# Kernel optimization log

Measured on AMD Instinct MI355X. Metric: run time of the kernel, lower is better.

Reference implementation:

```python
import jax, jax.numpy as jnp
import numpy as np

BS, HIST, H, W, NOBJ = 512, 3, 10, 10, 4
NSENT, TOK, DM = 3, 36, 768
EMB, FM, K, NL, ADIM = 256, 64, 2, 128, 5
LIN = FM * (H - (K - 1)) * (W - (K - 1))  # 64*9*9 = 5184
ATTN_SCALE = float(np.sqrt(EMB))  # 16.0


def setup_inputs() -> dict:
    key = jax.random.key(0)
    ks = jax.random.split(key, 24)
    g = lambda i, shape, s=0.02: jax.random.normal(ks[i], shape, dtype=jnp.float32) * s
    sprite_emb = g(0, (25, EMB), 1.0).at[0].set(0.0)  # padding_idx=0 -> zero row
    inp = {
        'state': jax.random.randint(ks[1], (BS, HIST, H, W, NOBJ), 0, 25, dtype=jnp.int32),
        'action': jax.random.randint(ks[2], (BS,), 0, ADIM, dtype=jnp.int32),
        'temb': jax.random.normal(ks[3], (BS, NSENT, TOK, DM), dtype=jnp.float32),
        'sprite_emb': sprite_emb,
        'conv_w': g(4, (K, K, HIST * EMB, FM)),  # HWIO
        'conv_b': g(5, (FM,)),
        'Wk': g(6, (DM, EMB)), 'bk': g(7, (EMB,)),
        'Wks': g(8, (DM, 1)), 'bks': g(9, (1,)),
        'Wv': g(10, (DM, EMB)), 'bv': g(11, (EMB,)),
        'Wvs': g(12, (DM, 1)), 'bvs': g(13, (1,)),
        'a1': g(14, (LIN, NL)), 'a1b': g(15, (NL,)),
        'a2': g(16, (NL, NL)), 'a2b': g(17, (NL,)),
        'a3': g(18, (NL, ADIM)), 'a3b': g(19, (ADIM,)),
        'v1': g(20, (LIN, NL)), 'v1b': g(21, (NL,)),
        'v2': g(22, (NL, NL)), 'v2b': g(23, (NL,)),
        'v3': jax.random.normal(jax.random.fold_in(key, 99), (NL, 1)) * 0.02,
        'v3b': jnp.zeros((1,), jnp.float32),
    }
    return inp


def _nonzero_mean(e):
    # e: [..., n, emb]; mean over rows that are nonzero (padding rows are all-zero)
    cnt = jnp.sum(jnp.sum(e, axis=-1) != 0, axis=-1, keepdims=True)
    return jnp.sum(e, axis=-2) / jnp.maximum(cnt, 1).astype(e.dtype)


def reference(state, action, temb, sprite_emb, conv_w, conv_b, Wk, bk, Wks, bks,
              Wv, bv, Wvs, bvs, a1, a1b, a2, a2b, a3, a3b, v1, v1b, v2, v2b, v3, v3b):
    lrelu = jax.nn.leaky_relu  # slope 0.01 matches torch default
    bs = state.shape[0]
    obj_state, avt_state = state[..., :-1], state[..., -1:]
    query = _nonzero_mean(sprite_emb[obj_state])   # [bs,hist,H,W,emb]
    avatar = _nonzero_mean(sprite_emb[avt_state])  # [bs,hist,H,W,emb]
    # text key/value: scaled token-softmax pooling over tokens (dim=2)
    k = (temb @ Wk + bk) * jax.nn.softmax(temb @ Wks + bks, axis=-2)
    k = jnp.sum(k, axis=2)                          # [bs,nsent,emb]
    v = (temb @ Wv + bv) * jax.nn.softmax(temb @ Wvs + bvs, axis=-2)
    v = jnp.sum(v, axis=2)                          # [bs,nsent,emb]
    # batch_attention
    q2 = query.reshape(bs, -1, EMB)                 # [bs, hist*H*W, emb]
    kq = jnp.einsum('bxe,bse->bxs', q2, k) / ATTN_SCALE
    wts = jax.nn.softmax(kq, axis=-1) * (kq != 0)
    wts = wts.reshape(bs, HIST, H, W, NSENT)
    # mean(weights[...,None]*value, dim=-2) == (w @ v) / nsent
    att = jnp.einsum('bthws,bse->bthwe', wts, v) / NSENT  # [bs,hist,H,W,emb]
    st = att.reshape(bs, H, W, -1)                  # fold hist into channels (768)
    av = avatar.reshape(bs, H, W, -1)
    st = (st + av) / 2.0                            # NHWC, C=768
    y = jax.lax.conv_general_dilated(st, conv_w, (1, 1), 'VALID',
                                     dimension_numbers=('NHWC', 'HWIO', 'NHWC')) + conv_b
    y = lrelu(y)                                    # [bs,9,9,64]
    y = jnp.transpose(y, (0, 3, 1, 2)).reshape(bs, -1)  # torch NCHW flatten order
    ha = lrelu(lrelu(y @ a1 + a1b) @ a2 + a2b)
    logits = ha @ a3 + a3b
    logp = jax.nn.log_softmax(logits, axis=-1)
    action_logprobs = jnp.take_along_axis(logp, action[:, None].astype(jnp.int32), axis=-1)[:, 0]
    entropy = -jnp.sum(jnp.exp(logp) * logp, axis=-1)
    hv = lrelu(lrelu(y @ v1 + v1b) @ v2 + v2b)
    state_value = (hv @ v3 + v3b)[:, 0]
    return action_logprobs, state_value, entropy
```

## Files before the change

kernel.cpp:

```cpp
#include <hip/hip_runtime.h>
#include <hip/hip_bf16.h>
#include <math.h>

constexpr int BS   = 512;
constexpr int DM   = 768;
constexpr int NBS  = 1536;
constexpr int NPOS = 300;
constexpr int LIN  = 5184;
constexpr int KSPLIT = 27, KCH = 192;

typedef __attribute__((ext_vector_type(8))) short bf16x8;
typedef __attribute__((ext_vector_type(4))) short s16x4;
typedef __attribute__((ext_vector_type(4))) float f32x4;

static __device__ __forceinline__ short f2bf(float f) {
    unsigned u = __float_as_uint(f);
    unsigned r = (u + 0x7FFFu + ((u >> 16) & 1u)) >> 16;
    return (short)r;
}

constexpr size_t OFF_P    = 0;
constexpr size_t OFF_C0   = 19200;
constexpr size_t OFF_FL   = 19264;
constexpr size_t OFF_RD   = 19328;
constexpr size_t OFF_DT   = 39296;
constexpr size_t OFF_W2T  = 77696;
constexpr size_t OFF_WVH  = 176000;
constexpr size_t OFF_WCT  = 274304;
constexpr size_t OFF_AB   = 569216;
constexpr size_t OFF_SK   = 1232768;
constexpr size_t OFF_SV   = 1288064;
constexpr size_t OFF_XVH  = 1343360;
constexpr size_t OFF_VW   = 1933184;
constexpr size_t OFF_YH   = 3112832;
constexpr size_t OFF_PART = 4439936;

__global__ __launch_bounds__(256) void kA_prep(
    const float* __restrict__ conv_w, const float* __restrict__ sprite,
    const float* __restrict__ bk, const float* __restrict__ Wk,
    const float* __restrict__ Wv, const float* __restrict__ bv,
    const float* __restrict__ a1, const float* __restrict__ v1,
    short* __restrict__ W2T, short* __restrict__ WVH, short* __restrict__ AB,
    float* __restrict__ P, float* __restrict__ RD,
    float* __restrict__ C0, int* __restrict__ FL)
{
    __shared__ float tile[64][65];
    int bx = blockIdx.x, tid = threadIdx.x;
    if (bx < 48) {
        int p = bx >> 2, cq = bx & 3;
        int t4 = p / 3, j = p - t4 * 3;
        int c0 = cq * 64;
        #pragma unroll
        for (int it = 0; it < 16; ++it) {
            int idx = it * 256 + tid; int ci = idx >> 6, f = idx & 63;
            tile[ci][f] = conv_w[(size_t)(t4 * 768 + j * 256 + c0 + ci) * 64 + f];
        }
        __syncthreads();
        #pragma unroll
        for (int it = 0; it < 16; ++it) {
            int idx = it * 256 + tid; int f = idx >> 6, ci = idx & 63;
            W2T[(size_t)((t4 * 3 + j) * 64 + f) * 256 + c0 + ci] = f2bf(tile[ci][f]);
        }
    } else if (bx < 96) {
        int id = bx - 48;
        int base = id * 4096 + tid * 16;
        #pragma unroll
        for (int q = 0; q < 4; ++q) {
            float4 v = *(const float4*)(Wv + base + q * 4);
            s16x4 h = { f2bf(v.x), f2bf(v.y), f2bf(v.z), f2bf(v.w) };
            *(s16x4*)(WVH + base + q * 4) = h;
        }
    } else if (bx < 420) {
        int id = bx - 96; int kt = id % 81, nt = id / 81;
        const float* src = (nt < 2) ? a1 : v1;
        int col0 = (nt & 1) * 64;
        #pragma unroll
        for (int it = 0; it < 16; ++it) {
            int idx = it * 256 + tid; int ki = idx >> 6, ni = idx & 63;
            tile[ki][ni] = src[(size_t)(kt * 64 + ki) * 128 + col0 + ni];
        }
        __syncthreads();
        #pragma unroll
        for (int it = 0; it < 16; ++it) {
            int idx = it * 256 + tid; int ni = idx >> 6, ki = idx & 63;
            AB[(size_t)(nt * 64 + ni) * 5184 + kt * 64 + ki] = f2bf(tile[ki][ni]);
        }
    } else if (bx < 495) {
        int g = (bx - 420) * 256 + tid; int o = g / 768, d = g - o * 768;
        const float* sp = sprite + o * 256;
        const float* wr = Wk + (size_t)d * 256;
        float s = 0.f;
        for (int c = 0; c < 256; ++c) s += sp[c] * wr[c];
        P[g] = s;
    } else if (bx < 573) {
        int g = (bx - 495) * 256 + tid;
        int o = g / 768, n = g - o * 768;
        int tap = n >> 6, f = n & 63; int t4 = tap / 3, j = tap - t4 * 3;
        const float* sp = (o < 25) ? (sprite + o * 256) : bv;
        float s = 0.f;
        for (int e = 0; e < 256; ++e)
            s += sp[e] * conv_w[(size_t)(t4 * 768 + j * 256 + e) * 64 + f];
        RD[g] = s;
    } else {
        if (tid < 25) {
            float s = 0.f, cc = 0.f;
            for (int c = 0; c < 256; ++c) {
                float e = sprite[tid * 256 + c];
                s += e; cc += e * bk[c];
            }
            FL[tid] = (s != 0.0f) ? 1 : 0;
            C0[tid] = cc;
        }
    }
}

__global__ __launch_bounds__(256) void kB1_scores(
    const float* __restrict__ temb, const float* __restrict__ Wks,
    const float* __restrict__ Wvs, float* __restrict__ SK, float* __restrict__ SV)
{
    int wid = threadIdx.x >> 6, lane = threadIdx.x & 63;
    int r = blockIdx.x * 4 + wid;
    const float4* row = (const float4*)temb + (size_t)r * 192;
    const float4* k4 = (const float4*)Wks;
    const float4* v4 = (const float4*)Wvs;
    float pk = 0.f, pv = 0.f;
    #pragma unroll
    for (int i = 0; i < 3; ++i) {
        int d4 = lane + 64 * i;
        float4 x = row[d4];
        float4 wk = k4[d4], wv = v4[d4];
        pk += x.x * wk.x + x.y * wk.y + x.z * wk.z + x.w * wk.w;
        pv += x.x * wv.x + x.y * wv.y + x.z * wv.z + x.w * wv.w;
    }
    #pragma unroll
    for (int off = 32; off; off >>= 1) {
        pk += __shfl_down(pk, off);
        pv += __shfl_down(pv, off);
    }
    if (lane == 0) { SK[r] = pk; SV[r] = pv; }
}

__global__ __launch_bounds__(256) void kB2_sum(
    const float* __restrict__ temb, const float* __restrict__ SK,
    const float* __restrict__ SV, const float* __restrict__ P,
    const float* __restrict__ C0, short* __restrict__ XVH, float* __restrict__ DT)
{
    __shared__ float swk[40], swv[40];
    __shared__ float xk[768], xv[768];
    int tid = threadIdx.x, wid = tid >> 6, lane = tid & 63;
    int bs = blockIdx.x;

    if (wid < 2) {
        const float* S = wid ? SV : SK;
        float s = (lane < 36) ? S[bs * 36 + lane] : -INFINITY;
        float m = s;
        #pragma unroll
        for (int off = 32; off; off >>= 1) m = fmaxf(m, __shfl_xor(m, off));
        float e = (lane < 36) ? expf(s - m) : 0.f;
        float z = e;
        #pragma unroll
        for (int off = 32; off; off >>= 1) z += __shfl_xor(z, off);
        float* dst = wid ? swv : swk;
        if (lane < 36) dst[lane] = e / z;
    }
    __syncthreads();

    int tl[3], dd[3];
    #pragma unroll
    for (int i = 0; i < 3; ++i) { int g = i * 256 + tid; tl[i] = g / 192; dd[i] = g % 192; }
    float4 accK[3], accV[3];
    #pragma unroll
    for (int i = 0; i < 3; ++i) {
        accK[i] = make_float4(0.f, 0.f, 0.f, 0.f);
        accV[i] = make_float4(0.f, 0.f, 0.f, 0.f);
    }
    const float4* row = (const float4*)temb + (size_t)bs * 6912;
    for (int g = 0; g < 9; ++g) {
        #pragma unroll
        for (int i = 0; i < 3; ++i) {
            float4 x = row[g * 768 + i * 256 + tid];
            float wk = swk[4 * g + tl[i]], wv = swv[4 * g + tl[i]];
            accK[i].x += wk * x.x; accK[i].y += wk * x.y;
            accK[i].z += wk * x.z; accK[i].w += wk * x.w;
            accV[i].x += wv * x.x; accV[i].y += wv * x.y;
            accV[i].z += wv * x.z; accV[i].w += wv * x.w;
        }
    }
    #pragma unroll
    for (int p = 0; p < 4; ++p) {
        #pragma unroll
        for (int i = 0; i < 3; ++i) if (tl[i] == p) {
            if (p == 0) {
                *(float4*)&xk[4 * dd[i]] = accK[i];
                *(float4*)&xv[4 * dd[i]] = accV[i];
            } else {
                float4 t0 = *(const float4*)&xk[4 * dd[i]];
                t0.x += accK[i].x; t0.y += accK[i].y; t0.z += accK[i].z; t0.w += accK[i].w;
                *(float4*)&xk[4 * dd[i]] = t0;
                float4 t1 = *(const float4*)&xv[4 * dd[i]];
                t1.x += accV[i].x; t1.y += accV[i].y; t1.z += accV[i].z; t1.w += accV[i].w;
                *(float4*)&xv[4 * dd[i]] = t1;
            }
        }
        __syncthreads();
    }
    if (tid < 192) {
        float4 vv = *(const float4*)&xv[4 * tid];
        s16x4 h = { f2bf(vv.x), f2bf(vv.y), f2bf(vv.z), f2bf(vv.w) };
        *(s16x4*)(XVH + (size_t)bs * 768 + 4 * tid) = h;
    }
    for (int o = wid; o < 25; o += 4) {
        const float* pr = P + o * 768;
        float s = 0.f;
        #pragma unroll
        for (int j = 0; j < 12; ++j) s += xk[lane + 64 * j] * pr[lane + 64 * j];
        #pragma unroll
        for (int off = 32; off; off >>= 1) s += __shfl_down(s, off);
        if (lane == 0) DT[bs * 25 + o] = s + C0[o];
    }
}

template<int BIAS, int OUTBF>
__global__ __launch_bounds__(256) void gemm_mfma(
    const short* __restrict__ A, const short* __restrict__ B,
    const float* __restrict__ bias, void* __restrict__ Cout,
    int K, int ldc, int klen, size_t czstride)
{
    __shared__ short As[64][40];
    __shared__ short Bs[64][40];
    int tid = threadIdx.x;
    int bm = blockIdx.x * 64, bn = blockIdx.y * 64;
    int wid = tid >> 6, lane = tid & 63;
    int wm = (wid >> 1) * 32, wn = (wid & 1) * 32;
    int l15 = lane & 15, lg = lane >> 4;

    f32x4 zero = {0.f, 0.f, 0.f, 0.f};
    f32x4 acc00 = zero, acc01 = zero, acc10 = zero, acc11 = zero;

    int srow = tid >> 2, kch = (tid & 3) * 8;
    const short* Ap = A + (size_t)(bm + srow) * K + kch + (size_t)blockIdx.z * klen;
    const short* Bp = B + (size_t)(bn + srow) * K + kch + (size_t)blockIdx.z * klen;

    for (int kt = 0; kt < klen; kt += 32) {
        bf16x8 aval = *(const bf16x8*)(Ap + kt);
        bf16x8 bval = *(const bf16x8*)(Bp + kt);
        *(bf16x8*)&As[srow][kch] = aval;
        *(bf16x8*)&Bs[srow][kch] = bval;
        __syncthreads();
        bf16x8 af0 = *(const bf16x8*)&As[wm + l15][lg * 8];
        bf16x8 af1 = *(const bf16x8*)&As[wm + 16 + l15][lg * 8];
        bf16x8 bg0 = *(const bf16x8*)&Bs[wn + l15][lg * 8];
        bf16x8 bg1 = *(const bf16x8*)&Bs[wn + 16 + l15][lg * 8];
        acc00 = __builtin_amdgcn_mfma_f32_16x16x32_bf16(af0, bg0, acc00, 0, 0, 0);
        acc01 = __builtin_amdgcn_mfma_f32_16x16x32_bf16(af0, bg1, acc01, 0, 0, 0);
        acc10 = __builtin_amdgcn_mfma_f32_16x16x32_bf16(af1, bg0, acc10, 0, 0, 0);
        acc11 = __builtin_amdgcn_mfma_f32_16x16x32_bf16(af1, bg1, acc11, 0, 0, 0);
        __syncthreads();
    }

    float* Cf = (float*)Cout + (size_t)blockIdx.z * czstride;
    short* Ch = (short*)Cout;
    #pragma unroll
    for (int i = 0; i < 2; ++i) {
        f32x4 arow0 = (i == 0) ? acc00 : acc10;
        f32x4 arow1 = (i == 0) ? acc01 : acc11;
        #pragma unroll
        for (int j = 0; j < 2; ++j) {
            f32x4 a = (j == 0) ? arow0 : arow1;
            int col = bn + wn + j * 16 + l15;
            float bb = BIAS ? bias[col] : 0.f;
            #pragma unroll
            for (int r = 0; r < 4; ++r) {
                int row = bm + wm + i * 16 + lg * 4 + r;
                float v = a[r] + bb;
                if (OUTBF) Ch[(size_t)row * ldc + col] = f2bf(v);
                else       Cf[(size_t)row * ldc + col] = v;
            }
        }
    }
}

__global__ __launch_bounds__(256) void k4_y(
    const int* __restrict__ state, const float* __restrict__ dt,
    const int* __restrict__ flags, const float* __restrict__ vW,
    const float* __restrict__ rowdot, const float* __restrict__ conv_b,
    short* __restrict__ y)
{
    int b = blockIdx.x, tid = threadIdx.x;
    __shared__ float s_vW[3 * 768];
    __shared__ float s_w[3][NPOS + 4];
    __shared__ int   s_avt[NPOS + 4];
    __shared__ float s_y[81 * 65];

    const float4* vs = (const float4*)(vW + (size_t)b * 3 * 768);
    float4* vd = (float4*)s_vW;
    for (int i = tid; i < 576; i += 256) vd[i] = vs[i];

    for (int code = tid; code < NPOS; code += 256) {
        const int* st = state + ((size_t)b * NPOS + code) * 4;
        int o0 = st[0], o1 = st[1], o2 = st[2], avi = st[3];
        int cnt = flags[o0] + flags[o1] + flags[o2];
        s_avt[code] = avi;
        float w0 = 0.f, w1 = 0.f, w2 = 0.f;
        if (cnt > 0) {
            const float* d0 = dt + (size_t)b * 75;
            float inv = 1.0f / (16.0f * (float)cnt);
            float q0 = (d0[o0]      + d0[o1]      + d0[o2])      * inv;
            float q1 = (d0[25 + o0] + d0[25 + o1] + d0[25 + o2]) * inv;
            float q2 = (d0[50 + o0] + d0[50 + o1] + d0[50 + o2]) * inv;
            float m = fmaxf(q0, fmaxf(q1, q2));
            float e0 = expf(q0 - m), e1 = expf(q1 - m), e2 = expf(q2 - m);
            float is = 1.0f / (6.0f * (e0 + e1 + e2));
            w0 = e0 * is; w1 = e1 * is; w2 = e2 * is;
        }
        s_w[0][code] = w0; s_w[1][code] = w1; s_w[2][code] = w2;
    }
    __syncthreads();

    int f = tid & 63;
    float cb = conv_b[f];
    for (int p = tid >> 6; p < 81; p += 4) {
        int oh = p / 9, ow = p - oh * 9;
        float acc = cb;
        #pragma unroll
        for (int kh = 0; kh < 2; ++kh)
        #pragma unroll
        for (int kw = 0; kw < 2; ++kw) {
            int bc = 3 * ((oh + kh) * 10 + (ow + kw));
            int tbase = ((kh * 2 + kw) * 3) * 64 + f;
            #pragma unroll
            for (int j = 0; j < 3; ++j) {
                int code = bc + j;
                int tf = tbase + j * 64;
                acc += s_w[0][code] * s_vW[tf]
                     + s_w[1][code] * s_vW[768 + tf]
                     + s_w[2][code] * s_vW[2 * 768 + tf];
                acc += 0.5f * rowdot[(size_t)s_avt[code] * 768 + tf];
            }
        }
        acc = acc > 0.f ? acc : 0.01f * acc;
        s_y[p * 65 + f] = acc;
    }
    __syncthreads();
    for (int i = tid; i < LIN; i += 256) {
        int ff = i / 81, pp = i - ff * 81;
        y[(size_t)b * LIN + i] = f2bf(s_y[pp * 65 + ff]);
    }
}

__global__ __launch_bounds__(128) void k7_heads(
    const float* __restrict__ PART, const float* __restrict__ a1b,
    const float* __restrict__ v1b, const int* __restrict__ action,
    const float* __restrict__ a2, const float* __restrict__ a2b,
    const float* __restrict__ a3, const float* __restrict__ a3b,
    const float* __restrict__ v2, const float* __restrict__ v2b,
    const float* __restrict__ v3, const float* __restrict__ v3b,
    float* __restrict__ out)
{
    int b = blockIdx.x, tid = threadIdx.x;
    __shared__ float h1a[128], h1v[128], h2a[128], red[128];
    __shared__ float lg[5];
    float sa0 = a1b[tid], sv0 = v1b[tid];
    const float* pb = PART + (size_t)b * 256;
    for (int z = 0; z < KSPLIT; ++z) {
        sa0 += pb[(size_t)z * (BS * 256) + tid];
        sv0 += pb[(size_t)z * (BS * 256) + 128 + tid];
    }
    h1a[tid] = sa0 > 0.f ? sa0 : 0.01f * sa0;
    h1v[tid] = sv0 > 0.f ? sv0 : 0.01f * sv0;
    __syncthreads();
    float sa = a2b[tid], sv = v2b[tid];
    for (int k = 0; k < 128; ++k) {
        sa += h1a[k] * a2[k * 128 + tid];
        sv += h1v[k] * v2[k * 128 + tid];
    }
    sa = sa > 0.f ? sa : 0.01f * sa;
    sv = sv > 0.f ? sv : 0.01f * sv;
    h2a[tid] = sa;
    red[tid] = sv * v3[tid];
    __syncthreads();
    for (int s = 64; s > 0; s >>= 1) {
        if (tid < s) red[tid] += red[tid + s];
        __syncthreads();
    }
    if (tid < 5) {
        float l = a3b[tid];
        for (int k = 0; k < 128; ++k) l += h2a[k] * a3[k * 5 + tid];
        lg[tid] = l;
    }
    __syncthreads();
    if (tid == 0) {
        float m = lg[0];
        for (int j2 = 1; j2 < 5; ++j2) m = fmaxf(m, lg[j2]);
        float se = 0.f;
        for (int j2 = 0; j2 < 5; ++j2) se += expf(lg[j2] - m);
        float lse = m + logf(se);
        int act = action[b];
        float ent = 0.f;
        for (int j2 = 0; j2 < 5; ++j2) {
            float lp = lg[j2] - lse;
            ent -= expf(lp) * lp;
        }
        out[b]        = lg[act] - lse;
        out[512 + b]  = red[0] + v3b[0];
        out[1024 + b] = ent;
    }
}

extern "C" void kernel_launch(void* const* d_in, const int* in_sizes, int n_in,
                              void* d_out, int out_size, void* d_ws, size_t ws_size,
                              hipStream_t stream)
{
    const int*   state  = (const int*)d_in[0];
    const int*   action = (const int*)d_in[1];
    const float* temb   = (const float*)d_in[2];
    const float* sprite = (const float*)d_in[3];
    const float* conv_w = (const float*)d_in[4];
    const float* conv_b = (const float*)d_in[5];
    const float* Wk     = (const float*)d_in[6];
    const float* bk     = (const float*)d_in[7];
    const float* Wks    = (const float*)d_in[8];
    const float* Wv     = (const float*)d_in[10];
    const float* bv     = (const float*)d_in[11];
    const float* Wvs    = (const float*)d_in[12];
    const float* a1     = (const float*)d_in[14];
    const float* a1b    = (const float*)d_in[15];
    const float* a2     = (const float*)d_in[16];
    const float* a2b    = (const float*)d_in[17];
    const float* a3     = (const float*)d_in[18];
    const float* a3b    = (const float*)d_in[19];
    const float* v1     = (const float*)d_in[20];
    const float* v1b    = (const float*)d_in[21];
    const float* v2     = (const float*)d_in[22];
    const float* v2b    = (const float*)d_in[23];
    const float* v3     = (const float*)d_in[24];
    const float* v3b    = (const float*)d_in[25];
    (void)in_sizes; (void)n_in; (void)out_size; (void)ws_size;

    float* ws  = (float*)d_ws;
    float* P   = ws + OFF_P;
    float* C0  = ws + OFF_C0;
    int*   FL  = (int*)(ws + OFF_FL);
    float* RD  = ws + OFF_RD;
    float* bvW2= RD + 25 * 768;
    float* DT  = ws + OFF_DT;
    short* W2T = (short*)(ws + OFF_W2T);
    short* WVH = (short*)(ws + OFF_WVH);
    short* WCT = (short*)(ws + OFF_WCT);
    short* AB  = (short*)(ws + OFF_AB);
    float* SK  = ws + OFF_SK;
    float* SV  = ws + OFF_SV;
    short* XVH = (short*)(ws + OFF_XVH);
    float* VW  = ws + OFF_VW;
    short* YH  = (short*)(ws + OFF_YH);
    float* PART= ws + OFF_PART;
    float* out = (float*)d_out;

    kA_prep<<<574, 256, 0, stream>>>(conv_w, sprite, bk, Wk, Wv, bv, a1, v1,
                                     W2T, WVH, AB, P, RD, C0, FL);
    gemm_mfma<0,1><<<dim3(12,12,1),256,0,stream>>>(W2T, WVH, nullptr, WCT, 256, 768, 256, 0);

    kB1_scores<<<13824, 256, 0, stream>>>(temb, Wks, Wvs, SK, SV);
    kB2_sum<<<NBS, 256, 0, stream>>>(temb, SK, SV, P, C0, XVH, DT);

    gemm_mfma<1,0><<<dim3(24,12,1),256,0,stream>>>(XVH, WCT, bvW2, VW, 768, 768, 768, 0);

    k4_y<<<BS, 256, 0, stream>>>(state, DT, FL, VW, RD, conv_b, YH);

    gemm_mfma<0,0><<<dim3(8,4,KSPLIT),256,0,stream>>>(YH, AB, nullptr, PART, 5184, 256, KCH, (size_t)BS*256);

    k7_heads<<<BS, 128, 0, stream>>>(PART, a1b, v1b, action, a2, a2b, a3, a3b,
                                     v2, v2b, v3, v3b, out);
}
```

Baseline: 136.8 us.

## Fuse text score and pooling into one LDS-staged pass, compute DT via MFMA

The separate score kernel and pooling kernel are merged into one 512-thread block per batch-sentence. Each block stages the 36x768 text embedding in LDS, so the large temb tensor is read from global memory once instead of twice. The weight-prep work is folded into the same launch as extra blocks. The key-sprite dot products (DT) become an extra row of blocks in an MFMA GEMM that also produces VW, which is now stored in bf16. The constant bias term C0 is dropped because it cancels in the sentence softmax. The split-K count for the final large GEMM also drops from 27 to 9, and the y kernel moves to 512 threads. The main trade-off is about 110KB of LDS per block, which limits occupancy to roughly one block per CU.

```diff
diff --git a/kernel.cpp b/kernel.cpp
--- a/kernel.cpp
+++ b/kernel.cpp
@@ -7,7 +7,7 @@
 constexpr int NBS  = 1536;
 constexpr int NPOS = 300;
 constexpr int LIN  = 5184;
-constexpr int KSPLIT = 27, KCH = 192;
+constexpr int KSPLIT = 9, KCH = 576;
 
 typedef __attribute__((ext_vector_type(8))) short bf16x8;
 typedef __attribute__((ext_vector_type(4))) short s16x4;
@@ -18,205 +18,174 @@
     unsigned r = (u + 0x7FFFu + ((u >> 16) & 1u)) >> 16;
     return (short)r;
 }
-
-constexpr size_t OFF_P    = 0;
-constexpr size_t OFF_C0   = 19200;
-constexpr size_t OFF_FL   = 19264;
-constexpr size_t OFF_RD   = 19328;
-constexpr size_t OFF_DT   = 39296;
-constexpr size_t OFF_W2T  = 77696;
-constexpr size_t OFF_WVH  = 176000;
-constexpr size_t OFF_WCT  = 274304;
-constexpr size_t OFF_AB   = 569216;
-constexpr size_t OFF_SK   = 1232768;
-constexpr size_t OFF_SV   = 1288064;
-constexpr size_t OFF_XVH  = 1343360;
-constexpr size_t OFF_VW   = 1933184;
-constexpr size_t OFF_YH   = 3112832;
-constexpr size_t OFF_PART = 4439936;
-
-__global__ __launch_bounds__(256) void kA_prep(
-    const float* __restrict__ conv_w, const float* __restrict__ sprite,
-    const float* __restrict__ bk, const float* __restrict__ Wk,
+static __device__ __forceinline__ float bf2f_lo(unsigned u) {
+    return __uint_as_float(u << 16);
+}
+static __device__ __forceinline__ float bf2f_hi(unsigned u) {
+    return __uint_as_float(u & 0xFFFF0000u);
+}
+
+constexpr size_t OFF_RD   = 0;
+constexpr size_t OFF_FL   = 19968;
+constexpr size_t OFF_DT   = 20032;
+constexpr size_t OFF_W2T  = 118336;
+constexpr size_t OFF_WVH  = 167488;
+constexpr size_t OFF_WCT  = 216640;
+constexpr size_t OFF_PH   = 511552;
+constexpr size_t OFF_AB   = 536128;
+constexpr size_t OFF_XKH  = 1199680;
+constexpr size_t OFF_XVH  = 1789504;
+constexpr size_t OFF_VWH  = 2379328;
+constexpr size_t OFF_YH   = 2969152;
+constexpr size_t OFF_PART = 4296256;
+
+__global__ __launch_bounds__(512) void k1_main(
+    const float* __restrict__ temb, const float* __restrict__ Wks,
+    const float* __restrict__ Wvs, const float* __restrict__ conv_w,
+    const float* __restrict__ sprite, const float* __restrict__ Wk,
     const float* __restrict__ Wv, const float* __restrict__ bv,
     const float* __restrict__ a1, const float* __restrict__ v1,
+    short* __restrict__ XKH, short* __restrict__ XVH,
     short* __restrict__ W2T, short* __restrict__ WVH, short* __restrict__ AB,
-    float* __restrict__ P, float* __restrict__ RD,
-    float* __restrict__ C0, int* __restrict__ FL)
-{
-    __shared__ float tile[64][65];
-    int bx = blockIdx.x, tid = threadIdx.x;
-    if (bx < 48) {
-        int p = bx >> 2, cq = bx & 3;
+    short* __restrict__ PH, float* __restrict__ RD, int* __restrict__ FL)
+{
+    __shared__ float buf[36 * 768];
+    __shared__ float sco[4][40];
+    int tid = threadIdx.x, bx = blockIdx.x;
+
+    if (bx < NBS) {
+        int bs = bx;
+        const float4* src4 = (const float4*)temb + (size_t)bs * 6912;
+        float4 r[14];
+        #pragma unroll
+        for (int c = 0; c < 14; ++c) {
+            int i = c * 512 + tid;
+            if (c < 13 || tid < 256) r[c] = src4[i];
+        }
+        #pragma unroll
+        for (int c = 0; c < 14; ++c) {
+            int i = c * 512 + tid;
+            if (c < 13 || tid < 256) *(float4*)&buf[4 * i] = r[c];
+        }
+        __syncthreads();
+        int w = tid >> 6, lane = tid & 63;
+        const float4* wk4 = (const float4*)Wks;
+        const float4* wv4 = (const float4*)Wvs;
+        for (int t = w; t < 36; t += 8) {
+            float pk = 0.f, pv = 0.f;
+            #pragma unroll
+            for (int rd = 0; rd < 3; ++rd) {
+                int i4 = rd * 64 + lane;
+                float4 x = *(const float4*)&buf[t * 768 + i4 * 4];
+                float4 a = wk4[i4], b = wv4[i4];
+                pk += x.x * a.x + x.y * a.y + x.z * a.z + x.w * a.w;
+                pv += x.x * b.x + x.y * b.y + x.z * b.z + x.w * b.w;
+            }
+            #pragma unroll
+            for (int off = 32; off; off >>= 1) {
+                pk += __shfl_down(pk, off);
+                pv += __shfl_down(pv, off);
+            }
+            if (lane == 0) { sco[0][t] = pk; sco[1][t] = pv; }
+        }
+        __syncthreads();
+        if (w < 2) {
+            float s = (lane < 36) ? sco[w][lane] : -INFINITY;
+            float m = s;
+            #pragma unroll
+            for (int off = 32; off; off >>= 1) m = fmaxf(m, __shfl_xor(m, off));
+            float e = (lane < 36) ? expf(s - m) : 0.f;
+            float z = e;
+            #pragma unroll
+            for (int off = 32; off; off >>= 1) z += __shfl_xor(z, off);
+            if (lane < 36) sco[2 + w][lane] = e / z;
+        }
+        __syncthreads();
+        if (tid < 384) {
+            float k0 = 0.f, k1v = 0.f, v0 = 0.f, v1v = 0.f;
+            #pragma unroll
+            for (int t = 0; t < 36; ++t) {
+                float2 x = *(const float2*)&buf[t * 768 + 2 * tid];
+                float wkt = sco[2][t], wvt = sco[3][t];
+                k0 += wkt * x.x; k1v += wkt * x.y;
+                v0 += wvt * x.x; v1v += wvt * x.y;
+            }
+            ushort2 hk = { (unsigned short)f2bf(k0), (unsigned short)f2bf(k1v) };
+            ushort2 hv = { (unsigned short)f2bf(v0), (unsigned short)f2bf(v1v) };
+            *(ushort2*)&XKH[(size_t)bs * 768 + 2 * tid] = hk;
+            *(ushort2*)&XVH[(size_t)bs * 768 + 2 * tid] = hv;
+        }
+        return;
+    }
+
+    int id = bx - NBS;
+    float (*tile)[65] = (float(*)[65])buf;
+    if (id < 48) {
+        int p = id >> 2, cq = id & 3;
         int t4 = p / 3, j = p - t4 * 3;
         int c0 = cq * 64;
         #pragma unroll
-        for (int it = 0; it < 16; ++it) {
-            int idx = it * 256 + tid; int ci = idx >> 6, f = idx & 63;
+        for (int it = 0; it < 8; ++it) {
+            int idx = it * 512 + tid; int ci = idx >> 6, f = idx & 63;
             tile[ci][f] = conv_w[(size_t)(t4 * 768 + j * 256 + c0 + ci) * 64 + f];
         }
         __syncthreads();
         #pragma unroll
-        for (int it = 0; it < 16; ++it) {
-            int idx = it * 256 + tid; int f = idx >> 6, ci = idx & 63;
+        for (int it = 0; it < 8; ++it) {
+            int idx = it * 512 + tid; int f = idx >> 6, ci = idx & 63;
             W2T[(size_t)((t4 * 3 + j) * 64 + f) * 256 + c0 + ci] = f2bf(tile[ci][f]);
         }
-    } else if (bx < 96) {
-        int id = bx - 48;
-        int base = id * 4096 + tid * 16;
-        #pragma unroll
-        for (int q = 0; q < 4; ++q) {
-            float4 v = *(const float4*)(Wv + base + q * 4);
+    } else if (id < 60) {
+        int b2 = id - 48;
+        #pragma unroll
+        for (int it = 0; it < 8; ++it) {
+            int i4 = b2 * 4096 + it * 512 + tid;
+            float4 v = ((const float4*)Wv)[i4];
             s16x4 h = { f2bf(v.x), f2bf(v.y), f2bf(v.z), f2bf(v.w) };
-            *(s16x4*)(WVH + base + q * 4) = h;
-        }
-    } else if (bx < 420) {
-        int id = bx - 96; int kt = id % 81, nt = id / 81;
+            *(s16x4*)&WVH[4 * i4] = h;
+        }
+    } else if (id < 384) {
+        int q = id - 60; int kt = q % 81, nt = q / 81;
         const float* src = (nt < 2) ? a1 : v1;
         int col0 = (nt & 1) * 64;
         #pragma unroll
-        for (int it = 0; it < 16; ++it) {
-            int idx = it * 256 + tid; int ki = idx >> 6, ni = idx & 63;
+        for (int it = 0; it < 8; ++it) {
+            int idx = it * 512 + tid; int ki = idx >> 6, ni = idx & 63;
             tile[ki][ni] = src[(size_t)(kt * 64 + ki) * 128 + col0 + ni];
         }
         __syncthreads();
         #pragma unroll
-        for (int it = 0; it < 16; ++it) {
-            int idx = it * 256 + tid; int ni = idx >> 6, ki = idx & 63;
+        for (int it = 0; it < 8; ++it) {
+            int idx = it * 512 + tid; int ni = idx >> 6, ki = idx & 63;
             AB[(size_t)(nt * 64 + ni) * 5184 + kt * 64 + ki] = f2bf(tile[ki][ni]);
         }
-    } else if (bx < 495) {
-        int g = (bx - 420) * 256 + tid; int o = g / 768, d = g - o * 768;
-        const float* sp = sprite + o * 256;
-        const float* wr = Wk + (size_t)d * 256;
-        float s = 0.f;
-        for (int c = 0; c < 256; ++c) s += sp[c] * wr[c];
-        P[g] = s;
-    } else if (bx < 573) {
-        int g = (bx - 495) * 256 + tid;
-        int o = g / 768, n = g - o * 768;
-        int tap = n >> 6, f = n & 63; int t4 = tap / 3, j = tap - t4 * 3;
-        const float* sp = (o < 25) ? (sprite + o * 256) : bv;
-        float s = 0.f;
-        for (int e = 0; e < 256; ++e)
-            s += sp[e] * conv_w[(size_t)(t4 * 768 + j * 256 + e) * 64 + f];
-        RD[g] = s;
+    } else if (id < 422) {
+        int g = (id - 384) * 512 + tid;
+        if (g < 19200) {
+            int o = g / 768, d = g - o * 768;
+            const float* sp = sprite + o * 256;
+            const float* wr = Wk + (size_t)d * 256;
+            float s = 0.f;
+            for (int c = 0; c < 256; ++c) s += sp[c] * wr[c];
+            PH[(size_t)o * 768 + d] = f2bf(s);
+        }
+    } else if (id < 461) {
+        int g = (id - 422) * 512 + tid;
+        if (g < 19968) {
+            int o = g / 768, n = g - o * 768;
+            int tap = n >> 6, f = n & 63; int t4 = tap / 3, j = tap - t4 * 3;
+            const float* sp = (o < 25) ? (sprite + o * 256) : bv;
+            float s = 0.f;
+            for (int e = 0; e < 256; ++e)
+                s += sp[e] * conv_w[(size_t)(t4 * 768 + j * 256 + e) * 64 + f];
+            RD[g] = s;
+        }
     } else {
         if (tid < 25) {
-            float s = 0.f, cc = 0.f;
-            for (int c = 0; c < 256; ++c) {
-                float e = sprite[tid * 256 + c];
-                s += e; cc += e * bk[c];
-            }
+            float s = 0.f;
+            for (int c = 0; c < 256; ++c) s += sprite[tid * 256 + c];
             FL[tid] = (s != 0.0f) ? 1 : 0;
-            C0[tid] = cc;
-        }
-    }
-}
-
-__global__ __launch_bounds__(256) void kB1_scores(
-    const float* __restrict__ temb, const float* __restrict__ Wks,
-    const float* __restrict__ Wvs, float* __restrict__ SK, float* __restrict__ SV)
-{
-    int wid = threadIdx.x >> 6, lane = threadIdx.x & 63;
-    int r = blockIdx.x * 4 + wid;
-    const float4* row = (const float4*)temb + (size_t)r * 192;
-    const float4* k4 = (const float4*)Wks;
-    const float4* v4 = (const float4*)Wvs;
-    float pk = 0.f, pv = 0.f;
-    #pragma unroll
-    for (int i = 0; i < 3; ++i) {
-        int d4 = lane + 64 * i;
-        float4 x = row[d4];
-        float4 wk = k4[d4], wv = v4[d4];
-        pk += x.x * wk.x + x.y * wk.y + x.z * wk.z + x.w * wk.w;
-        pv += x.x * wv.x + x.y * wv.y + x.z * wv.z + x.w * wv.w;
-    }
-    #pragma unroll
-    for (int off = 32; off; off >>= 1) {
-        pk += __shfl_down(pk, off);
-        pv += __shfl_down(pv, off);
-    }
-    if (lane == 0) { SK[r] = pk; SV[r] = pv; }
-}
-
-__global__ __launch_bounds__(256) void kB2_sum(
-    const float* __restrict__ temb, const float* __restrict__ SK,
-    const float* __restrict__ SV, const float* __restrict__ P,
-    const float* __restrict__ C0, short* __restrict__ XVH, float* __restrict__ DT)
-{
-    __shared__ float swk[40], swv[40];
-    __shared__ float xk[768], xv[768];
-    int tid = threadIdx.x, wid = tid >> 6, lane = tid & 63;
-    int bs = blockIdx.x;
-
-    if (wid < 2) {
-        const float* S = wid ? SV : SK;
-        float s = (lane < 36) ? S[bs * 36 + lane] : -INFINITY;
-        float m = s;
-        #pragma unroll
-        for (int off = 32; off; off >>= 1) m = fmaxf(m, __shfl_xor(m, off));
-        float e = (lane < 36) ? expf(s - m) : 0.f;
-        float z = e;
-        #pragma unroll
-        for (int off = 32; off; off >>= 1) z += __shfl_xor(z, off);
-        float* dst = wid ? swv : swk;
-        if (lane < 36) dst[lane] = e / z;
-    }
-    __syncthreads();
-
-    int tl[3], dd[3];
-    #pragma unroll
-    for (int i = 0; i < 3; ++i) { int g = i * 256 + tid; tl[i] = g / 192; dd[i] = g % 192; }
-    float4 accK[3], accV[3];
-    #pragma unroll
-    for (int i = 0; i < 3; ++i) {
-        accK[i] = make_float4(0.f, 0.f, 0.f, 0.f);
-        accV[i] = make_float4(0.f, 0.f, 0.f, 0.f);
-    }
-    const float4* row = (const float4*)temb + (size_t)bs * 6912;
-    for (int g = 0; g < 9; ++g) {
-        #pragma unroll
-        for (int i = 0; i < 3; ++i) {
-            float4 x = row[g * 768 + i * 256 + tid];
-            float wk = swk[4 * g + tl[i]], wv = swv[4 * g + tl[i]];
-            accK[i].x += wk * x.x; accK[i].y += wk * x.y;
-            accK[i].z += wk * x.z; accK[i].w += wk * x.w;
-            accV[i].x += wv * x.x; accV[i].y += wv * x.y;
-            accV[i].z += wv * x.z; accV[i].w += wv * x.w;
-        }
-    }
-    #pragma unroll
-    for (int p = 0; p < 4; ++p) {
-        #pragma unroll
-        for (int i = 0; i < 3; ++i) if (tl[i] == p) {
-            if (p == 0) {
-                *(float4*)&xk[4 * dd[i]] = accK[i];
-                *(float4*)&xv[4 * dd[i]] = accV[i];
-            } else {
-                float4 t0 = *(const float4*)&xk[4 * dd[i]];
-                t0.x += accK[i].x; t0.y += accK[i].y; t0.z += accK[i].z; t0.w += accK[i].w;
-                *(float4*)&xk[4 * dd[i]] = t0;
-                float4 t1 = *(const float4*)&xv[4 * dd[i]];
-                t1.x += accV[i].x; t1.y += accV[i].y; t1.z += accV[i].z; t1.w += accV[i].w;
-                *(float4*)&xv[4 * dd[i]] = t1;
-            }
-        }
-        __syncthreads();
-    }
-    if (tid < 192) {
-        float4 vv = *(const float4*)&xv[4 * tid];
-        s16x4 h = { f2bf(vv.x), f2bf(vv.y), f2bf(vv.z), f2bf(vv.w) };
-        *(s16x4*)(XVH + (size_t)bs * 768 + 4 * tid) = h;
-    }
-    for (int o = wid; o < 25; o += 4) {
-        const float* pr = P + o * 768;
-        float s = 0.f;
-        #pragma unroll
-        for (int j = 0; j < 12; ++j) s += xk[lane + 64 * j] * pr[lane + 64 * j];
-        #pragma unroll
-        for (int off = 32; off; off >>= 1) s += __shfl_down(s, off);
-        if (lane == 0) DT[bs * 25 + o] = s + C0[o];
+        }
     }
 }
 
@@ -280,9 +249,68 @@
     }
 }
 
-__global__ __launch_bounds__(256) void k4_y(
+__global__ __launch_bounds__(256) void k3_vwdt(
+    const short* __restrict__ XVH, const short* __restrict__ WCT,
+    const float* __restrict__ bvW2, short* __restrict__ VWH,
+    const short* __restrict__ XKH, const short* __restrict__ PH,
+    float* __restrict__ DT)
+{
+    __shared__ short As[64][40];
+    __shared__ short Bs[64][40];
+    int tid = threadIdx.x;
+    bool isdt = (blockIdx.y == 12);
+    const short* A = isdt ? XKH : XVH;
+    const short* B = isdt ? PH  : WCT;
+    int bm = blockIdx.x * 64, bn = isdt ? 0 : blockIdx.y * 64;
+    int wid = tid >> 6, lane = tid & 63;
+    int wm = (wid >> 1) * 32, wn = (wid & 1) * 32;
+    int l15 = lane & 15, lg = lane >> 4;
+
+    f32x4 zero = {0.f, 0.f, 0.f, 0.f};
+    f32x4 acc00 = zero, acc01 = zero, acc10 = zero, acc11 = zero;
+
+    int srow = tid >> 2, kch = (tid & 3) * 8;
+    const short* Ap = A + (size_t)(bm + srow) * 768 + kch;
+    const short* Bp = B + (size_t)(bn + srow) * 768 + kch;
+
+    for (int kt = 0; kt < 768; kt += 32) {
+        bf16x8 aval = *(const bf16x8*)(Ap + kt);
+        bf16x8 bval = *(const bf16x8*)(Bp + kt);
+        *(bf16x8*)&As[srow][kch] = aval;
+        *(bf16x8*)&Bs[srow][kch] = bval;
+        __syncthreads();
+        bf16x8 af0 = *(const bf16x8*)&As[wm + l15][lg * 8];
+        bf16x8 af1 = *(const bf16x8*)&As[wm + 16 + l15][lg * 8];
+        bf16x8 bg0 = *(const bf16x8*)&Bs[wn + l15][lg * 8];
+        bf16x8 bg1 = *(const bf16x8*)&Bs[wn + 16 + l15][lg * 8];
+        acc00 = __builtin_amdgcn_mfma_f32_16x16x32_bf16(af0, bg0, acc00, 0, 0, 0);
+        acc01 = __builtin_amdgcn_mfma_f32_16x16x32_bf16(af0, bg1, acc01, 0, 0, 0);
+        acc10 = __builtin_amdgcn_mfma_f32_16x16x32_bf16(af1, bg0, acc10, 0, 0, 0);
+        acc11 = __builtin_amdgcn_mfma_f32_16x16x32_bf16(af1, bg1, acc11, 0, 0, 0);
+        __syncthreads();
+    }
+
+    #pragma unroll
+    for (int i = 0; i < 2; ++i) {
+        f32x4 arow0 = (i == 0) ? acc00 : acc10;
+        f32x4 arow1 = (i == 0) ? acc01 : acc11;
+        #pragma unroll
+        for (int j = 0; j < 2; ++j) {
+            f32x4 a = (j == 0) ? arow0 : arow1;
+            int col = bn + wn + j * 16 + l15;
+            #pragma unroll
+            for (int r = 0; r < 4; ++r) {
+                int row = bm + wm + i * 16 + lg * 4 + r;
+                if (isdt) DT[(size_t)row * 64 + col] = a[r];
+                else      VWH[(size_t)row * 768 + col] = f2bf(a[r] + bvW2[col]);
+            }
+        }
+    }
+}
+
+__global__ __launch_bounds__(512) void k4_y(
     const int* __restrict__ state, const float* __restrict__ dt,
-    const int* __restrict__ flags, const float* __restrict__ vW,
+    const int* __restrict__ flags, const short* __restrict__ VWH,
     const float* __restrict__ rowdot, const float* __restrict__ conv_b,
     short* __restrict__ y)
 {
@@ -292,22 +320,25 @@
     __shared__ int   s_avt[NPOS + 4];
     __shared__ float s_y[81 * 65];
 
-    const float4* vs = (const float4*)(vW + (size_t)b * 3 * 768);
-    float4* vd = (float4*)s_vW;
-    for (int i = tid; i < 576; i += 256) vd[i] = vs[i];
-
-    for (int code = tid; code < NPOS; code += 256) {
+    const unsigned* vr = (const unsigned*)(VWH + (size_t)b * 3 * 768);
+    for (int i = tid; i < 1152; i += 512) {
+        unsigned u = vr[i];
+        s_vW[2 * i]     = bf2f_lo(u);
+        s_vW[2 * i + 1] = bf2f_hi(u);
+    }
+
+    for (int code = tid; code < NPOS; code += 512) {
         const int* st = state + ((size_t)b * NPOS + code) * 4;
         int o0 = st[0], o1 = st[1], o2 = st[2], avi = st[3];
         int cnt = flags[o0] + flags[o1] + flags[o2];
         s_avt[code] = avi;
         float w0 = 0.f, w1 = 0.f, w2 = 0.f;
         if (cnt > 0) {
-            const float* d0 = dt + (size_t)b * 75;
+            const float* d0 = dt + (size_t)b * 192;
             float inv = 1.0f / (16.0f * (float)cnt);
-            float q0 = (d0[o0]      + d0[o1]      + d0[o2])      * inv;
-            float q1 = (d0[25 + o0] + d0[25 + o1] + d0[25 + o2]) * inv;
-            float q2 = (d0[50 + o0] + d0[50 + o1] + d0[50 + o2]) * inv;
+            float q0 = (d0[o0]       + d0[o1]       + d0[o2])       * inv;
+            float q1 = (d0[64 + o0]  + d0[64 + o1]  + d0[64 + o2])  * inv;
+            float q2 = (d0[128 + o0] + d0[128 + o1] + d0[128 + o2]) * inv;
             float m = fmaxf(q0, fmaxf(q1, q2));
             float e0 = expf(q0 - m), e1 = expf(q1 - m), e2 = expf(q2 - m);
             float is = 1.0f / (6.0f * (e0 + e1 + e2));
@@ -319,7 +350,7 @@
 
     int f = tid & 63;
     float cb = conv_b[f];
-    for (int p = tid >> 6; p < 81; p += 4) {
+    for (int p = tid >> 6; p < 81; p += 8) {
         int oh = p / 9, ow = p - oh * 9;
         float acc = cb;
         #pragma unroll
@@ -342,13 +373,13 @@
         s_y[p * 65 + f] = acc;
     }
     __syncthreads();
-    for (int i = tid; i < LIN; i += 256) {
+    for (int i = tid; i < LIN; i += 512) {
         int ff = i / 81, pp = i - ff * 81;
         y[(size_t)b * LIN + i] = f2bf(s_y[pp * 65 + ff]);
     }
 }
 
-__global__ __launch_bounds__(128) void k7_heads(
+__global__ __launch_bounds__(128) void k6_heads(
     const float* __restrict__ PART, const float* __restrict__ a1b,
     const float* __restrict__ v1b, const int* __restrict__ action,
     const float* __restrict__ a2, const float* __restrict__ a2b,
@@ -418,7 +449,6 @@
     const float* conv_w = (const float*)d_in[4];
     const float* conv_b = (const float*)d_in[5];
     const float* Wk     = (const float*)d_in[6];
-    const float* bk     = (const float*)d_in[7];
     const float* Wks    = (const float*)d_in[8];
     const float* Wv     = (const float*)d_in[10];
     const float* bv     = (const float*)d_in[11];
@@ -438,37 +468,28 @@
     (void)in_sizes; (void)n_in; (void)out_size; (void)ws_size;
 
     float* ws  = (float*)d_ws;
-    float* P   = ws + OFF_P;
-    float* C0  = ws + OFF_C0;
-    int*   FL  = (int*)(ws + OFF_FL);
     float* RD  = ws + OFF_RD;
     float* bvW2= RD + 25 * 768;
+    int*   FL  = (int*)(ws + OFF_FL);
     float* DT  = ws + OFF_DT;
     short* W2T = (short*)(ws + OFF_W2T);
     short* WVH = (short*)(ws + OFF_WVH);
     short* WCT = (short*)(ws + OFF_WCT);
+    short* PH  = (short*)(ws + OFF_PH);
     short* AB  = (short*)(ws + OFF_AB);
-    float* SK  = ws + OFF_SK;
-    float* SV  = ws + OFF_SV;
+    short* XKH = (short*)(ws + OFF_XKH);
     short* XVH = (short*)(ws + OFF_XVH);
-    float* VW  = ws + OFF_VW;
+    short* VWH = (short*)(ws + OFF_VWH);
     short* YH  = (short*)(ws + OFF_YH);
     float* PART= ws + OFF_PART;
     float* out = (float*)d_out;
 
-    kA_prep<<<574, 256, 0, stream>>>(conv_w, sprite, bk, Wk, Wv, bv, a1, v1,
-                                     W2T, WVH, AB, P, RD, C0, FL);
+    k1_main<<<1998, 512, 0, stream>>>(temb, Wks, Wvs, conv_w, sprite, Wk, Wv, bv,
+                                      a1, v1, XKH, XVH, W2T, WVH, AB, PH, RD, FL);
     gemm_mfma<0,1><<<dim3(12,12,1),256,0,stream>>>(W2T, WVH, nullptr, WCT, 256, 768, 256, 0);
-
-    kB1_scores<<<13824, 256, 0, stream>>>(temb, Wks, Wvs, SK, SV);
-    kB2_sum<<<NBS, 256, 0, stream>>>(temb, SK, SV, P, C0, XVH, DT);
-
-    gemm_mfma<1,0><<<dim3(24,12,1),256,0,stream>>>(XVH, WCT, bvW2, VW, 768, 768, 768, 0);
-
-    k4_y<<<BS, 256, 0, stream>>>(state, DT, FL, VW, RD, conv_b, YH);
-
+    k3_vwdt<<<dim3(24,13,1),256,0,stream>>>(XVH, WCT, bvW2, VWH, XKH, PH, DT);
+    k4_y<<<BS, 512, 0, stream>>>(state, DT, FL, VWH, RD, conv_b, YH);
     gemm_mfma<0,0><<<dim3(8,4,KSPLIT),256,0,stream>>>(YH, AB, nullptr, PART, 5184, 256, KCH, (size_t)BS*256);
-
-    k7_heads<<<BS, 128, 0, stream>>>(PART, a1b, v1b, action, a2, a2b, a3, a3b,
+    k6_heads<<<BS, 128, 0, stream>>>(PART, a1b, v1b, action, a2, a2b, a3, a3b,
                                      v2, v2b, v3, v3b, out);
 }
```

After: 159.6 us. +16.7%, slower.
